# Kernel optimization log

Measured on AMD Instinct MI355X. Metric: run time of the kernel, lower is better.

## Reference

```python
import jax, jax.numpy as jnp
import numpy as np

DIM = 1024
HEADS = 16
HEAD_DIM = DIM // HEADS
SCALE = HEAD_DIM ** -0.5
LN_EPS = 1e-5


def setup_inputs() -> dict:
    key = jax.random.key(0)
    ks = jax.random.split(key, 8)
    B, N = 2, 2048
    s = 0.02
    return {
        "embedding1": jax.random.normal(ks[0], (B, N, DIM), jnp.float32),
        "embedding2": jax.random.normal(ks[1], (B, N, DIM), jnp.float32),
        "Wqkv": jax.random.normal(ks[2], (DIM, 3 * DIM), jnp.float32) * s,
        "bqkv": jnp.zeros((3 * DIM,), jnp.float32),
        "Wout": jax.random.normal(ks[3], (DIM, DIM), jnp.float32) * s,
        "bout": jnp.zeros((DIM,), jnp.float32),
        "gamma": jnp.ones((DIM,), jnp.float32),
        "beta": jnp.zeros((DIM,), jnp.float32),
    }


def _layernorm(x, gamma, beta):
    mu = jnp.mean(x, axis=-1, keepdims=True)
    var = jnp.mean(jnp.square(x - mu), axis=-1, keepdims=True)
    return (x - mu) * jax.lax.rsqrt(var + LN_EPS) * gamma + beta


def _qkv(x, Wqkv, bqkv):
    B, N, _ = x.shape
    qkv = (x @ Wqkv + bqkv).reshape(B, N, 3, HEADS, HEAD_DIM)
    return qkv[:, :, 0], qkv[:, :, 1], qkv[:, :, 2]  # each [B,N,H,D]


def _cross_attn(q, k, v):
    # q: [B,N,H,D], k/v: [B,S,H,D]
    scores = jnp.einsum("bnhd,bshd->bhns", q, k) * SCALE
    attn = jax.nn.softmax(scores, axis=-1)
    out = jnp.einsum("bhns,bshd->bnhd", attn, v)
    B, N = out.shape[0], out.shape[1]
    return out.reshape(B, N, DIM)


def reference(embedding1, embedding2, Wqkv, bqkv, Wout, bout, gamma, beta):
    q1, k1, v1 = _qkv(embedding1, Wqkv, bqkv)
    q2, k2, v2 = _qkv(embedding2, Wqkv, bqkv)
    attn1 = _cross_attn(q1, k2, v2)
    attn2 = _cross_attn(q2, k1, v1)
    out1 = _layernorm(embedding1 + attn1 @ Wout + bout, gamma, beta)
    out2 = _layernorm(embedding2 + attn2 @ Wout + bout, gamma, beta)
    return (out1, out2)
```

## Files before the change

kernel.cpp:

```cpp
#include <hip/hip_runtime.h>
#include <stdint.h>
#include <stddef.h>

#define DIM 1024
#define HEADS 16
#define HDIM 64
#define NTOK 2048

typedef __attribute__((ext_vector_type(8))) __bf16 bf16x8;
typedef __attribute__((ext_vector_type(4))) float f32x4;
typedef __attribute__((ext_vector_type(16))) float f32x16;
typedef __attribute__((ext_vector_type(4))) short short4v;
typedef __attribute__((ext_vector_type(4))) uint32_t u32x4;

__device__ __forceinline__ short f2bs(float f) {
  uint32_t u = __builtin_bit_cast(uint32_t, f);
  uint32_t r = (u + 0x7FFFu + ((u >> 16) & 1u)) >> 16;
  return (short)r;
}

__device__ __forceinline__ float bs2f(short s) {
  return __builtin_bit_cast(float, (uint32_t)((uint16_t)s) << 16);
}

__device__ __forceinline__ uint32_t cvtpk(float lo, float hi) {
  uint32_t r;
  asm("v_cvt_pk_bf16_f32 %0, %1, %2" : "=v"(r) : "v"(lo), "v"(hi));
  return r;
}

__device__ __forceinline__ f32x4 MFMA(bf16x8 a, bf16x8 b, f32x4 c) {
  return __builtin_amdgcn_mfma_f32_16x16x32_bf16(a, b, c, 0, 0, 0);
}
__device__ __forceinline__ f32x16 MFMA32(bf16x8 a, bf16x8 b, f32x16 c) {
  return __builtin_amdgcn_mfma_f32_32x32x16_bf16(a, b, c, 0, 0, 0);
}

__device__ __forceinline__ void gl_lds16(const void* g, void* l) {
  __builtin_amdgcn_global_load_lds(
      (const __attribute__((address_space(1))) void*)g,
      (__attribute__((address_space(3))) void*)l, 16, 0, 0);
}

__global__ __launch_bounds__(256) void cast_embs(const float4* __restrict__ e1,
                                                 const float4* __restrict__ e2,
                                                 short* __restrict__ X) {
  int i = blockIdx.x * 256 + threadIdx.x;
  const int half4 = (4096 * 1024) / 4;
  float4 v = (i < half4) ? e1[i] : e2[i - half4];
  short4v o;
  o.x = f2bs(v.x); o.y = f2bs(v.y); o.z = f2bs(v.z); o.w = f2bs(v.w);
  *(short4v*)&X[(size_t)i * 4] = o;
}

__global__ __launch_bounds__(256) void transpose_cast(const float* __restrict__ W,
                                                      short* __restrict__ Wt,
                                                      int R, int C) {
  __shared__ float tile[32][33];
  int tx = threadIdx.x, ty = threadIdx.y;
  int c0 = blockIdx.x * 32, r0 = blockIdx.y * 32;
#pragma unroll
  for (int i = 0; i < 32; i += 8)
    tile[ty + i][tx] = W[(size_t)(r0 + ty + i) * C + c0 + tx];
  __syncthreads();
#pragma unroll
  for (int i = 0; i < 32; i += 8)
    Wt[(size_t)(c0 + ty + i) * R + r0 + tx] = f2bs(tile[tx][ty + i]);
}

template <int EPI>
__global__ __launch_bounds__(256, 2) void gemm_bt(
    const short* __restrict__ A, const short* __restrict__ Bt, int K,
    const float* __restrict__ bias,
    const float* __restrict__ e1, const float* __restrict__ e2,
    short* __restrict__ oq, short* __restrict__ okk, short* __restrict__ ovt,
    short* __restrict__ oy) {
  __shared__ short lA[128 * 64];
  __shared__ short lB[128 * 64];
  int tid = threadIdx.x;
  int l = tid & 63, w = tid >> 6;
  int wr = w >> 1, wc = w & 1;
  int row0 = blockIdx.x * 128, col0 = blockIdx.y * 128;
  f32x4 acc[4][4] = {};

  for (int kk = 0; kk < K; kk += 64) {
#pragma unroll
    for (int i = 0; i < 4; i++) {
      int f = i * 256 + tid;
      int r = f >> 3, cb = (f & 7) * 8;
      gl_lds16(A + (size_t)(row0 + r) * K + kk + cb, (char*)lA + (size_t)f * 16);
      gl_lds16(Bt + (size_t)(col0 + r) * K + kk + cb, (char*)lB + (size_t)f * 16);
    }
    __syncthreads();
    bf16x8 af[2][4], bfr[2][4];
#pragma unroll
    for (int k2 = 0; k2 < 2; k2++) {
#pragma unroll
      for (int mi = 0; mi < 4; mi++)
        af[k2][mi] = *(const bf16x8*)&lA[(wr * 64 + mi * 16 + (l & 15)) * 64 + k2 * 32 + (l >> 4) * 8];
#pragma unroll
      for (int ni = 0; ni < 4; ni++)
        bfr[k2][ni] = *(const bf16x8*)&lB[(wc * 64 + ni * 16 + (l & 15)) * 64 + k2 * 32 + (l >> 4) * 8];
    }
#pragma unroll
    for (int k2 = 0; k2 < 2; k2++)
#pragma unroll
      for (int mi = 0; mi < 4; mi++)
#pragma unroll
        for (int ni = 0; ni < 4; ni++)
          acc[mi][ni] = MFMA(af[k2][mi], bfr[k2][ni], acc[mi][ni]);
    __syncthreads();
  }

#pragma unroll
  for (int mi = 0; mi < 4; mi++) {
#pragma unroll
    for (int ni = 0; ni < 4; ni++) {
#pragma unroll
      for (int r = 0; r < 4; r++) {
        int grow = row0 + wr * 64 + mi * 16 + (l >> 4) * 4 + r;
        int gcol = col0 + wc * 64 + ni * 16 + (l & 15);
        float v = acc[mi][ni][r] + bias[gcol];
        if (EPI == 0) {
          int t = gcol >> 10, rem = gcol & 1023;
          int h = rem >> 6, d = rem & 63;
          int e = grow >> 12, b = (grow >> 11) & 1, n = grow & 2047;
          size_t ebh = (size_t)((e * 2 + b) * 16 + h) * (NTOK * HDIM);
          if (t == 0) {
            oq[ebh + (size_t)n * HDIM + d] = f2bs(v * 0.18033688f);
          } else if (t == 1) {
            int ks = d >> 4, hi2 = (d >> 3) & 1, j = d & 7;
            int tt = n >> 6, rr = n & 63, h2 = rr >> 5, lo = rr & 31;
            okk[ebh + (((size_t)(tt * 8 + ks * 2 + h2)) * 64 + hi2 * 32 + lo) * 8 + j] = f2bs(v);
          } else {
            int tt = n >> 6, rr = n & 63;
            int ks = rr >> 4, hi2 = (rr >> 3) & 1, j = rr & 7;
            int h2 = d >> 5, lo = d & 31;
            ovt[ebh + (((size_t)(tt * 8 + ks * 2 + h2)) * 64 + hi2 * 32 + lo) * 8 + j] = f2bs(v);
          }
        } else {
          float res = (grow < 4096) ? e1[(size_t)grow * DIM + gcol]
                                    : e2[(size_t)(grow - 4096) * DIM + gcol];
          oy[(size_t)grow * DIM + gcol] = f2bs(v + res);
        }
      }
    }
  }
}

__global__ __launch_bounds__(64, 2) void attn_kernel(
    const short* __restrict__ qbuf, const short* __restrict__ kfb,
    const short* __restrict__ vfb, short* __restrict__ X2) {
  int phys = blockIdx.x;
  int work = (phys & 7) * 256 + (phys >> 3);
  int qw = work & 31;
  int inst = work >> 5;
  int h = inst & 15, b = (inst >> 4) & 1, a = inst >> 5;
  int l = threadIdx.x;
  int lo5 = l & 31, hi = l >> 5;

  size_t qo = (size_t)((a * 2 + b) * 16 + h) * (NTOK * HDIM);
  size_t ko = (size_t)(((a ^ 1) * 2 + b) * 16 + h) * (NTOK * HDIM);
  const short* Q = qbuf + qo;
  const short* Kf = kfb + ko;
  const short* Vf = vfb + ko;
  int qrowA = qw * 64 + lo5;
  int qrowB = qrowA + 32;

  bf16x8 qfA[4], qfB[4];
#pragma unroll
  for (int ks = 0; ks < 4; ks++) {
    qfA[ks] = *(const bf16x8*)&Q[(size_t)qrowA * HDIM + hi * 8 + ks * 16];
    qfB[ks] = *(const bf16x8*)&Q[(size_t)qrowB * HDIM + hi * 8 + ks * 16];
  }

  f32x16 oA0 = {}, oA1 = {}, oB0 = {}, oB1 = {};
  float lsA = 0.f, lsB = 0.f;

  bf16x8 ka[8], va[8];

#define LOADF(dst, buf, t)                                                   \
  {                                                                          \
    const short* _p = &buf[((size_t)(t) * 8) * 512 + l * 8];                 \
    _Pragma("unroll") for (int fi = 0; fi < 8; fi++)                         \
        dst[fi] = *(const bf16x8*)&_p[fi * 512];                             \
  }

#define QKBLK(s0, s1, qf)                                                    \
  {                                                                          \
    __builtin_amdgcn_s_setprio(1);                                           \
    _Pragma("unroll") for (int ks = 0; ks < 4; ks++) {                       \
      s0 = MFMA32(ka[2 * ks], qf[ks], s0);                                   \
      s1 = MFMA32(ka[2 * ks + 1], qf[ks], s1);                               \
    }                                                                        \
    __builtin_amdgcn_s_setprio(0);                                           \
  }

#define SOFTPV(s0, s1, oo0, oo1, ls)                                         \
  {                                                                          \
    _Pragma("unroll") for (int i = 0; i < 16; i++) {                         \
      s0[i] = exp2f(s0[i]);                                                  \
      s1[i] = exp2f(s1[i]);                                                  \
    }                                                                        \
    {                                                                        \
      float rt[16];                                                          \
      _Pragma("unroll") for (int i = 0; i < 16; i++) rt[i] = s0[i] + s1[i];  \
      _Pragma("unroll") for (int sd = 8; sd >= 1; sd >>= 1)                  \
          _Pragma("unroll") for (int i = 0; i < sd; i++) rt[i] += rt[i + sd];\
      ls += rt[0];                                                           \
    }                                                                        \
    bf16x8 pf[4];                                                            \
    _Pragma("unroll") for (int ks = 0; ks < 4; ks++) {                       \
      const int rb = (ks & 1) * 8;                                           \
      uint32_t A0, A1, B0, B1;                                               \
      if (ks < 2) {                                                          \
        A0 = cvtpk(s0[rb + 0], s0[rb + 1]);                                  \
        A1 = cvtpk(s0[rb + 2], s0[rb + 3]);                                  \
        B0 = cvtpk(s0[rb + 4], s0[rb + 5]);                                  \
        B1 = cvtpk(s0[rb + 6], s0[rb + 7]);                                  \
      } else {                                                               \
        A0 = cvtpk(s1[rb + 0], s1[rb + 1]);                                  \
        A1 = cvtpk(s1[rb + 2], s1[rb + 3]);                                  \
        B0 = cvtpk(s1[rb + 4], s1[rb + 5]);                                  \
        B1 = cvtpk(s1[rb + 6], s1[rb + 7]);                                  \
      }                                                                      \
      asm("v_permlane32_swap_b32 %0, %1" : "+v"(A0), "+v"(B0));              \
      asm("v_permlane32_swap_b32 %0, %1" : "+v"(A1), "+v"(B1));              \
      u32x4 fw; fw.x = A0; fw.y = A1; fw.z = B0; fw.w = B1;                  \
      pf[ks] = __builtin_bit_cast(bf16x8, fw);                               \
    }                                                                        \
    __builtin_amdgcn_s_setprio(1);                                           \
    _Pragma("unroll") for (int ks = 0; ks < 4; ks++) {                       \
      oo0 = MFMA32(va[2 * ks], pf[ks], oo0);                                 \
      oo1 = MFMA32(va[2 * ks + 1], pf[ks], oo1);                             \
    }                                                                        \
    __builtin_amdgcn_s_setprio(0);                                           \
  }

  LOADF(ka, Kf, 0);
  LOADF(va, Vf, 0);
  for (int t = 0; t < 32; t++) {
    f32x16 sA0 = {}, sA1 = {};
    QKBLK(sA0, sA1, qfA);
    SOFTPV(sA0, sA1, oA0, oA1, lsA);
    f32x16 sB0 = {}, sB1 = {};
    QKBLK(sB0, sB1, qfB);
    LOADF(ka, Kf, (t + 1) & 31);
    SOFTPV(sB0, sB1, oB0, oB1, lsB);
    LOADF(va, Vf, (t + 1) & 31);
  }

  lsA += __shfl_xor(lsA, 32);
  lsB += __shfl_xor(lsB, 32);
  float invA = 1.f / lsA, invB = 1.f / lsB;
  size_t obaseA = (size_t)(a * 4096 + b * 2048 + qrowA) * DIM + h * HDIM;
  size_t obaseB = (size_t)(a * 4096 + b * 2048 + qrowB) * DIM + h * HDIM;
#pragma unroll
  for (int g = 0; g < 4; g++) {
    short4v s4;
    s4.x = f2bs(oA0[4 * g + 0] * invA);
    s4.y = f2bs(oA0[4 * g + 1] * invA);
    s4.z = f2bs(oA0[4 * g + 2] * invA);
    s4.w = f2bs(oA0[4 * g + 3] * invA);
    *(short4v*)&X2[obaseA + 8 * g + 4 * hi] = s4;
    s4.x = f2bs(oA1[4 * g + 0] * invA);
    s4.y = f2bs(oA1[4 * g + 1] * invA);
    s4.z = f2bs(oA1[4 * g + 2] * invA);
    s4.w = f2bs(oA1[4 * g + 3] * invA);
    *(short4v*)&X2[obaseA + 32 + 8 * g + 4 * hi] = s4;
    s4.x = f2bs(oB0[4 * g + 0] * invB);
    s4.y = f2bs(oB0[4 * g + 1] * invB);
    s4.z = f2bs(oB0[4 * g + 2] * invB);
    s4.w = f2bs(oB0[4 * g + 3] * invB);
    *(short4v*)&X2[obaseB + 8 * g + 4 * hi] = s4;
    s4.x = f2bs(oB1[4 * g + 0] * invB);
    s4.y = f2bs(oB1[4 * g + 1] * invB);
    s4.z = f2bs(oB1[4 * g + 2] * invB);
    s4.w = f2bs(oB1[4 * g + 3] * invB);
    *(short4v*)&X2[obaseB + 32 + 8 * g + 4 * hi] = s4;
  }
#undef LOADF
#undef QKBLK
#undef SOFTPV
}

__global__ __launch_bounds__(256) void ln_kernel(const short* __restrict__ Y,
                                                 const float* __restrict__ gamma,
                                                 const float* __restrict__ beta,
                                                 float* __restrict__ out) {
  int row = blockIdx.x, t = threadIdx.x;
  const short4v v4 = *(const short4v*)&Y[(size_t)row * DIM + t * 4];
  float vx = bs2f(v4.x), vy = bs2f(v4.y), vz = bs2f(v4.z), vw = bs2f(v4.w);
  float s = vx + vy + vz + vw;
  float s2 = vx * vx + vy * vy + vz * vz + vw * vw;
#pragma unroll
  for (int d = 1; d < 64; d <<= 1) { s += __shfl_xor(s, d); s2 += __shfl_xor(s2, d); }
  __shared__ float sb[8];
  int w = t >> 6, l = t & 63;
  if (l == 0) { sb[w] = s; sb[4 + w] = s2; }
  __syncthreads();
  s = sb[0] + sb[1] + sb[2] + sb[3];
  s2 = sb[4] + sb[5] + sb[6] + sb[7];
  float mu = s * (1.f / DIM);
  float var = s2 * (1.f / DIM) - mu * mu;
  float rr = rsqrtf(var + 1e-5f);
  const float4 g = *(const float4*)&gamma[t * 4];
  const float4 bb = *(const float4*)&beta[t * 4];
  float4 ov;
  ov.x = (vx - mu) * rr * g.x + bb.x;
  ov.y = (vy - mu) * rr * g.y + bb.y;
  ov.z = (vz - mu) * rr * g.z + bb.z;
  ov.w = (vw - mu) * rr * g.w + bb.w;
  *(float4*)&out[(size_t)row * DIM + t * 4] = ov;
}

extern "C" void kernel_launch(void* const* d_in, const int* in_sizes, int n_in,
                              void* d_out, int out_size, void* d_ws, size_t ws_size,
                              hipStream_t stream) {
  const float* e1 = (const float*)d_in[0];
  const float* e2 = (const float*)d_in[1];
  const float* Wqkv = (const float*)d_in[2];
  const float* bqkv = (const float*)d_in[3];
  const float* Wout = (const float*)d_in[4];
  const float* bout = (const float*)d_in[5];
  const float* gamma = (const float*)d_in[6];
  const float* beta = (const float*)d_in[7];

  char* p = (char*)d_ws;
  short* Xbf   = (short*)p;
  short* Wqkvt = (short*)(p + 16777216);
  short* Woutt = (short*)(p + 23068672);
  short* qbf   = (short*)(p + 25165824);
  short* kbf   = (short*)(p + 41943040);
  short* vtf   = (short*)(p + 58720256);
  short* Yres  = (short*)(p + 25165824);
  short* X2    = Xbf;
  float* out   = (float*)d_out;

  cast_embs<<<8192, 256, 0, stream>>>((const float4*)e1, (const float4*)e2, Xbf);
  transpose_cast<<<dim3(3072 / 32, 1024 / 32), dim3(32, 8), 0, stream>>>(Wqkv, Wqkvt, 1024, 3072);
  transpose_cast<<<dim3(1024 / 32, 1024 / 32), dim3(32, 8), 0, stream>>>(Wout, Woutt, 1024, 1024);
  gemm_bt<0><<<dim3(64, 24), 256, 0, stream>>>(Xbf, Wqkvt, 1024, bqkv,
                                               nullptr, nullptr, qbf, kbf, vtf, nullptr);
  attn_kernel<<<2048, 64, 0, stream>>>(qbf, kbf, vtf, X2);
  gemm_bt<1><<<dim3(64, 8), 256, 0, stream>>>(X2, Woutt, 1024, bout,
                                              e1, e2, nullptr, nullptr, nullptr, Yres);
  ln_kernel<<<8192, 256, 0, stream>>>(Yres, gamma, beta, out);
}
```

Before: 328.9 us.

## Split attention KV loop across two waves per block and merge in LDS

Each attention block grows from one to two wavefronts. Each wave handles half of the 32 KV tiles for the same 64 query rows. The second wave writes its partial output accumulators and row sums to shared memory, and the first wave adds them in before normalizing and storing. The aim is to double the number of resident waves and hide latency in a kernel that previously ran one wave per block. The cost is extra shared-memory traffic, a block barrier, and a merge that is only correct if the softmax uses no per-wave running max.

```diff
diff --git a/kernel.cpp b/kernel.cpp
--- a/kernel.cpp
+++ b/kernel.cpp
@@ -148,7 +148,7 @@
   }
 }
 
-__global__ __launch_bounds__(64, 2) void attn_kernel(
+__global__ __launch_bounds__(128, 2) void attn_kernel(
     const short* __restrict__ qbuf, const short* __restrict__ kfb,
     const short* __restrict__ vfb, short* __restrict__ X2) {
   int phys = blockIdx.x;
@@ -156,7 +156,9 @@
   int qw = work & 31;
   int inst = work >> 5;
   int h = inst & 15, b = (inst >> 4) & 1, a = inst >> 5;
-  int l = threadIdx.x;
+  int tid = threadIdx.x;
+  int w = tid >> 6;
+  int l = tid & 63;
   int lo5 = l & 31, hi = l >> 5;
 
   size_t qo = (size_t)((a * 2 + b) * 16 + h) * (NTOK * HDIM);
@@ -237,17 +239,44 @@
     __builtin_amdgcn_s_setprio(0);                                           \
   }
 
-  LOADF(ka, Kf, 0);
-  LOADF(va, Vf, 0);
-  for (int t = 0; t < 32; t++) {
+  const int tbeg = w << 4;
+  LOADF(ka, Kf, tbeg);
+  LOADF(va, Vf, tbeg);
+  for (int ti = 0; ti < 16; ti++) {
     f32x16 sA0 = {}, sA1 = {};
     QKBLK(sA0, sA1, qfA);
     SOFTPV(sA0, sA1, oA0, oA1, lsA);
     f32x16 sB0 = {}, sB1 = {};
     QKBLK(sB0, sB1, qfB);
-    LOADF(ka, Kf, (t + 1) & 31);
+    LOADF(ka, Kf, tbeg + ((ti + 1) & 15));
     SOFTPV(sB0, sB1, oB0, oB1, lsB);
-    LOADF(va, Vf, (t + 1) & 31);
+    LOADF(va, Vf, tbeg + ((ti + 1) & 15));
+  }
+
+  __shared__ float mO[64][65];
+  __shared__ float mls[2][64];
+  if (w == 1) {
+#pragma unroll
+    for (int i = 0; i < 16; i++) {
+      mO[l][i]      = oA0[i];
+      mO[l][16 + i] = oA1[i];
+      mO[l][32 + i] = oB0[i];
+      mO[l][48 + i] = oB1[i];
+    }
+    mls[0][l] = lsA;
+    mls[1][l] = lsB;
+  }
+  __syncthreads();
+  if (w == 1) return;
+
+  lsA += mls[0][l];
+  lsB += mls[1][l];
+#pragma unroll
+  for (int i = 0; i < 16; i++) {
+    oA0[i] += mO[l][i];
+    oA1[i] += mO[l][16 + i];
+    oB0[i] += mO[l][32 + i];
+    oB1[i] += mO[l][48 + i];
   }
 
   lsA += __shfl_xor(lsA, 32);
@@ -342,7 +371,7 @@
   transpose_cast<<<dim3(1024 / 32, 1024 / 32), dim3(32, 8), 0, stream>>>(Wout, Woutt, 1024, 1024);
   gemm_bt<0><<<dim3(64, 24), 256, 0, stream>>>(Xbf, Wqkvt, 1024, bqkv,
                                                nullptr, nullptr, qbf, kbf, vtf, nullptr);
-  attn_kernel<<<2048, 64, 0, stream>>>(qbf, kbf, vtf, X2);
+  attn_kernel<<<2048, 128, 0, stream>>>(qbf, kbf, vtf, X2);
   gemm_bt<1><<<dim3(64, 8), 256, 0, stream>>>(X2, Woutt, 1024, bout,
                                               e1, e2, nullptr, nullptr, nullptr, Yres);
   ln_kernel<<<8192, 256, 0, stream>>>(Yres, gamma, beta, out);
```

Result: slower. 347.8 us (+5.7%).
